# Kernel tuning notes

Hardware: AMD Instinct MI355X
Metric: run time of the kernel (lower is better)

Reference implementation:

```python
import jax, jax.numpy as jnp
import numpy as np

B, N, D = 4, 4096, 256

def setup_inputs() -> dict:
    key = jax.random.key(0)
    k1, = jax.random.split(key, 1)
    x = jax.random.normal(k1, (B, N, D), dtype=jnp.float32)
    attn_mask = jnp.ones((B, 1, N), dtype=jnp.int32)
    pad_mask = jnp.ones((B, 1, N), dtype=jnp.int32)
    return {"x": x, "attn_mask": attn_mask, "pad_mask": pad_mask, "dim_": D}

def reference(x, attn_mask, pad_mask, dim_):
    # adj is None -> scores = x @ x^T / sqrt(d)
    scale = jnp.sqrt(jnp.asarray(x.shape[-1], x.dtype))
    scores = jnp.einsum('bnd,bmd->bnm', x, x) / scale  # [B, N, N]
    # NOTE: original calls non-in-place masked_fill and discards the result,
    # so pad_mask / attn_mask have no effect on the output (faithful).
    prob = jax.nn.softmax(scores, axis=-1)
    # dropout is identity in inference mode
    return jnp.einsum('bnm,bmd->bnd', prob, x)
```

## Files before the change

### kernel.cpp

```cpp
#include <hip/hip_runtime.h>

typedef __attribute__((ext_vector_type(8))) short short8;
typedef __attribute__((ext_vector_type(4))) float f32x4;
typedef __attribute__((ext_vector_type(4))) unsigned int u32x4;

#define NTOK 4096
#define DIM  256
#define P_STRIDE 72
#define TILE_ELEMS 32768

__device__ __forceinline__ unsigned pack2bf(float a, float b) {
  unsigned ua = __builtin_bit_cast(unsigned, a) + 0x8000u;
  unsigned ub = __builtin_bit_cast(unsigned, b) + 0x8000u;
  return __builtin_amdgcn_perm(ub, ua, 0x07060302u);
}

__global__ __launch_bounds__(256, 4)
void prep_kernel(const float* __restrict__ X, unsigned short* __restrict__ Img) {
  __shared__ __align__(16) unsigned short rowbf[8 * 256];
  const int b    = blockIdx.x & 3;
  const int sub  = blockIdx.x >> 2;
  const int t    = sub >> 3;
  const int part = sub & 7;
  const int tid  = threadIdx.x;
  const float* src = X + ((size_t)b * NTOK + t * 64 + part * 8) * DIM;
  unsigned short* dst = Img + ((size_t)(b * 64 + t)) * TILE_ELEMS;
  {
    const int r = tid >> 5;
    const int c = tid & 31;
    const float* s = src + r * DIM + c * 8;
    f32x4 f0 = *(const f32x4*)s;
    f32x4 f1 = *(const f32x4*)(s + 4);
    union { unsigned u[4]; u32x4 v; } p;
    p.u[0] = pack2bf(f0[0], f0[1]);
    p.u[1] = pack2bf(f0[2], f0[3]);
    p.u[2] = pack2bf(f1[0], f1[1]);
    p.u[3] = pack2bf(f1[2], f1[3]);
    const int gr = part * 8 + r;
    *(u32x4*)(dst + gr * 256 + ((c ^ (gr & 7)) << 3)) = p.v;
    *(u32x4*)(&rowbf[r * 256 + c * 8]) = p.v;
  }
  __syncthreads();
  {
    const int d = tid;
    union { unsigned short s[8]; u32x4 v; } p;
    #pragma unroll
    for (int i = 0; i < 8; ++i) p.s[i] = rowbf[i * 256 + d];
    *(u32x4*)(dst + 16384 + part * 2048 + d * 8) = p.v;
  }
}

__device__ __forceinline__ void pv_reg(const unsigned short* __restrict__ pr,
                                       const short8 (&bv)[2][4],
                                       f32x4 (&o)[2][4],
                                       int qh, int quad, int ln) {
  #pragma unroll
  for (int ks = 0; ks < 2; ++ks) {
    const int pos = (ks * 4 + quad) ^ ((ln >> 3) << 1);
    short8 ap[2];
    #pragma unroll
    for (int s = 0; s < 2; ++s)
      ap[s] = *(const short8*)(&pr[(qh * 32 + s * 16 + ln) * P_STRIDE + (pos << 3)]);
    #pragma unroll
    for (int s = 0; s < 2; ++s)
      #pragma unroll
      for (int dt = 0; dt < 4; ++dt)
        o[s][dt] = __builtin_amdgcn_mfma_f32_16x16x32_bf16(ap[s], bv[ks][dt], o[s][dt], 0, 0, 0);
  }
}

__global__ __launch_bounds__(512, 1)
void fa_kernel(const unsigned short* __restrict__ Img, float* __restrict__ Out) {
  __shared__ __align__(16) unsigned short ksb[2][16384];
  __shared__ __align__(16) unsigned short pb[2][64 * P_STRIDE];
  __shared__ float lbuf[64][4];

  const int tid  = threadIdx.x;
  const int b    = blockIdx.x & 3;
  const int qblk = blockIdx.x >> 2;
  const int wave = tid >> 6;
  const int lane = tid & 63;
  const int ln   = lane & 15;
  const int quad = lane >> 4;
  const int swz  = ln & 7;
  const int qh   = wave & 1;
  const int role = wave >> 1;

  const unsigned short* imgb  = Img + (size_t)b * 64 * TILE_ELEMS;
  const char*           imgbc = (const char*)imgb;

  short8 aQ[2][8];
  #pragma unroll
  for (int s = 0; s < 2; ++s) {
    const unsigned short* qrow =
        imgb + (size_t)qblk * TILE_ELEMS + (qh * 32 + s * 16 + ln) * 256;
    #pragma unroll
    for (int ds = 0; ds < 8; ++ds)
      aQ[s][ds] = *(const short8*)(qrow + (((ds * 4 + quad) ^ swz) << 3));
  }

  f32x4 o[2][4];
  #pragma unroll
  for (int s = 0; s < 2; ++s)
    #pragma unroll
    for (int dt = 0; dt < 4; ++dt) o[s][dt] = (f32x4)(0.0f);
  float lrow[2][4] = {{0.f,0.f,0.f,0.f},{0.f,0.f,0.f,0.f}};

  const float c2 = 0.0901684400f;

  const int pwPos = ((role * 2 + (ln >> 3)) ^ ((quad >> 1) << 1)) << 3;
  const int pwCol = ln & 7;

  const char* gK = imgbc + (size_t)wave * 4096 + (size_t)lane * 16;
  #pragma unroll
  for (int i = 0; i < 4; ++i)
    __builtin_amdgcn_global_load_lds(
        (const __attribute__((address_space(1))) unsigned*)(gK + i * 1024),
        (__attribute__((address_space(3))) unsigned*)(&ksb[0][wave * 2048 + i * 512]),
        16, 0, 0);

  const unsigned short* ktg = imgb + 16384 + (size_t)quad * 2048 + (role * 64 + ln) * 8;

  short8 bvE[2][4];
  short8 bvO[2][4];

  auto iter = [&](int t, short8 (&bvLd)[2][4], short8 (&bvUs)[2][4],
                  bool doPV) __attribute__((always_inline)) {
    __syncthreads();
    const int buf = t & 1;

    if (t < 63) {
      const char* g = gK + (size_t)(t + 1) * 65536;
      unsigned short* l = &ksb[buf ^ 1][wave * 2048];
      #pragma unroll
      for (int i = 0; i < 4; ++i)
        __builtin_amdgcn_global_load_lds(
            (const __attribute__((address_space(1))) unsigned*)(g + i * 1024),
            (__attribute__((address_space(3))) unsigned*)(l + i * 512),
            16, 0, 0);
    }

    {
      const unsigned short* kt = ktg + (size_t)t * TILE_ELEMS;
      #pragma unroll
      for (int ks = 0; ks < 2; ++ks)
        #pragma unroll
        for (int dt = 0; dt < 4; ++dt)
          bvLd[ks][dt] = *(const short8*)(kt + ks * 8192 + dt * 128);
    }

    f32x4 sf0 = (f32x4)(0.0f), sf1 = (f32x4)(0.0f);
    {
      const unsigned short* krow = &ksb[buf][(role * 16 + ln) * 256];
      #pragma unroll
      for (int ds = 0; ds < 8; ++ds) {
        short8 bk = *(const short8*)(krow + (((ds * 4 + quad) ^ swz) << 3));
        sf0 = __builtin_amdgcn_mfma_f32_16x16x32_bf16(aQ[0][ds], bk, sf0, 0, 0, 0);
        sf1 = __builtin_amdgcn_mfma_f32_16x16x32_bf16(aQ[1][ds], bk, sf1, 0, 0, 0);
      }
    }

    unsigned pd0[4], pd1[4];
    #pragma unroll
    for (int j = 0; j < 4; ++j) {
      float p0 = __builtin_amdgcn_exp2f(sf0[j] * c2);
      float p1 = __builtin_amdgcn_exp2f(sf1[j] * c2);
      lrow[0][j] += p0;
      lrow[1][j] += p1;
      unsigned q0 = __builtin_bit_cast(unsigned, p0);
      unsigned q1 = __builtin_bit_cast(unsigned, p1);
      unsigned n0 = (unsigned)__builtin_amdgcn_mov_dpp((int)q0, 0xB1, 0xF, 0xF, true);
      unsigned n1 = (unsigned)__builtin_amdgcn_mov_dpp((int)q1, 0xB1, 0xF, 0xF, true);
      pd0[j] = pack2bf(__builtin_bit_cast(float, q0), __builtin_bit_cast(float, n0));
      pd1[j] = pack2bf(__builtin_bit_cast(float, q1), __builtin_bit_cast(float, n1));
    }

    if (doPV)
      pv_reg(pb[buf ^ 1], bvUs, o, qh, quad, ln);

    if ((ln & 1) == 0) {
      unsigned short* pw = pb[buf];
      #pragma unroll
      for (int j = 0; j < 4; ++j) {
        const int r0 = qh * 32 + quad * 4 + j;
        *(unsigned*)(&pw[r0 * P_STRIDE + pwPos + pwCol]) = pd0[j];
        *(unsigned*)(&pw[(r0 + 16) * P_STRIDE + pwPos + pwCol]) = pd1[j];
      }
    }
  };

  iter(0, bvE, bvO, false);
  #pragma unroll 1
  for (int tt = 1; tt < 63; tt += 2) {
    iter(tt, bvO, bvE, true);
    iter(tt + 1, bvE, bvO, true);
  }
  iter(63, bvO, bvE, true);

  __syncthreads();
  pv_reg(pb[1], bvO, o, qh, quad, ln);

  #pragma unroll
  for (int off = 1; off < 16; off <<= 1)
    #pragma unroll
    for (int s = 0; s < 2; ++s)
      #pragma unroll
      for (int j = 0; j < 4; ++j)
        lrow[s][j] += __shfl_xor(lrow[s][j], off, 64);
  if (ln == 0) {
    #pragma unroll
    for (int s = 0; s < 2; ++s)
      #pragma unroll
      for (int j = 0; j < 4; ++j)
        lbuf[qh * 32 + s * 16 + quad * 4 + j][role] = lrow[s][j];
  }
  __syncthreads();

  #pragma unroll
  for (int s = 0; s < 2; ++s) {
    float* outp = Out + (size_t)(b * NTOK + qblk * 64 + qh * 32 + s * 16) * DIM + role * 64;
    #pragma unroll
    for (int j = 0; j < 4; ++j) {
      const int row = s * 16 + quad * 4 + j;
      f32x4 lv = *(const f32x4*)lbuf[qh * 32 + row];
      const float rl = 1.0f / (lv[0] + lv[1] + lv[2] + lv[3]);
      #pragma unroll
      for (int dt = 0; dt < 4; ++dt)
        outp[(size_t)(quad * 4 + j) * DIM + dt * 16 + ln] = o[s][dt][j] * rl;
    }
  }
}

extern "C" void kernel_launch(void* const* d_in, const int* in_sizes, int n_in,
                              void* d_out, int out_size, void* d_ws, size_t ws_size,
                              hipStream_t stream) {
  const float* X = (const float*)d_in[0];
  float* Out = (float*)d_out;
  unsigned short* Img = (unsigned short*)d_ws;
  (void)in_sizes; (void)n_in; (void)out_size; (void)ws_size;
  hipLaunchKernelGGL(prep_kernel, dim3(2048), dim3(256), 0, stream, X, Img);
  hipLaunchKernelGGL(fa_kernel, dim3(256), dim3(512), 0, stream, Img, Out);
}
```

Measured before the change: 166.3 us.

## Specialize waves into QK/softmax producers and PV consumers

Result: no change. 163.4 us (-1.8%).

```diff
diff --git a/kernel.cpp b/kernel.cpp
--- a/kernel.cpp
+++ b/kernel.cpp
@@ -50,24 +50,84 @@
   }
 }
 
-__device__ __forceinline__ void pv_reg(const unsigned short* __restrict__ pr,
-                                       const short8 (&bv)[2][4],
-                                       f32x4 (&o)[2][4],
-                                       int qh, int quad, int ln) {
-  #pragma unroll
-  for (int ks = 0; ks < 2; ++ks) {
-    const int pos = (ks * 4 + quad) ^ ((ln >> 3) << 1);
-    short8 ap[2];
-    #pragma unroll
-    for (int s = 0; s < 2; ++s)
-      ap[s] = *(const short8*)(&pr[(qh * 32 + s * 16 + ln) * P_STRIDE + (pos << 3)]);
-    #pragma unroll
-    for (int s = 0; s < 2; ++s)
-      #pragma unroll
-      for (int dt = 0; dt < 4; ++dt)
-        o[s][dt] = __builtin_amdgcn_mfma_f32_16x16x32_bf16(ap[s], bv[ks][dt], o[s][dt], 0, 0, 0);
-  }
-}
+#define FA_STEP(T, VLD, VUS)                                                   \
+  {                                                                            \
+    const int t_ = (T);                                                        \
+    __syncthreads();                                                           \
+    const int buf_ = t_ & 1;                                                   \
+    if (!isQK) {                                                               \
+      if (t_ < 63) {                                                           \
+        const char* g = gK + (size_t)(t_ + 1) * 65536;                         \
+        unsigned short* l = &ksb[buf_ ^ 1][role * 4096];                       \
+        _Pragma("unroll")                                                      \
+        for (int i = 0; i < 8; ++i)                                            \
+          __builtin_amdgcn_global_load_lds(                                    \
+              (const __attribute__((address_space(1))) unsigned*)(g + i*1024), \
+              (__attribute__((address_space(3))) unsigned*)(l + i*512),        \
+              16, 0, 0);                                                       \
+      }                                                                        \
+      {                                                                        \
+        const unsigned short* vt = vtg + (size_t)t_ * TILE_ELEMS;              \
+        _Pragma("unroll")                                                      \
+        for (int ks = 0; ks < 2; ++ks)                                         \
+          _Pragma("unroll")                                                    \
+          for (int dt = 0; dt < 4; ++dt)                                       \
+            u[(VLD) + ks * 4 + dt] = __builtin_bit_cast(f32x4,                 \
+                *(const short8*)(vt + (ks * 4 + quad) * 2048 + dt * 128));     \
+      }                                                                        \
+      if (t_ > 0) {                                                            \
+        const unsigned short* prd = pb[buf_ ^ 1];                              \
+        _Pragma("unroll")                                                      \
+        for (int ks = 0; ks < 2; ++ks) {                                       \
+          const int pos = (ks * 4 + quad) ^ ((ln >> 3) << 1);                  \
+          _Pragma("unroll")                                                    \
+          for (int s = 0; s < 4; ++s) {                                        \
+            short8 ap = *(const short8*)(                                      \
+                &prd[(s * 16 + ln) * P_STRIDE + (pos << 3)]);                  \
+            _Pragma("unroll")                                                  \
+            for (int dt = 0; dt < 4; ++dt)                                     \
+              u[s * 4 + dt] = __builtin_amdgcn_mfma_f32_16x16x32_bf16(         \
+                  ap, __builtin_bit_cast(short8, u[(VUS) + ks * 4 + dt]),      \
+                  u[s * 4 + dt], 0, 0, 0);                                     \
+          }                                                                    \
+        }                                                                      \
+      }                                                                        \
+    } else {                                                                   \
+      const unsigned short* krow = &ksb[buf_][(role * 16 + ln) * 256];         \
+      f32x4 sf[4];                                                             \
+      _Pragma("unroll")                                                        \
+      for (int s = 0; s < 4; ++s) sf[s] = (f32x4)(0.0f);                       \
+      _Pragma("unroll")                                                        \
+      for (int ds = 0; ds < 8; ++ds) {                                         \
+        short8 bk = *(const short8*)(krow + (((ds * 4 + quad) ^ swz) << 3));   \
+        _Pragma("unroll")                                                      \
+        for (int s = 0; s < 4; ++s)                                            \
+          sf[s] = __builtin_amdgcn_mfma_f32_16x16x32_bf16(                     \
+              __builtin_bit_cast(short8, u[s * 8 + ds]), bk, sf[s], 0, 0, 0);  \
+      }                                                                        \
+      unsigned pd[4][4];                                                       \
+      _Pragma("unroll")                                                        \
+      for (int s = 0; s < 4; ++s)                                              \
+        _Pragma("unroll")                                                      \
+        for (int j = 0; j < 4; ++j) {                                          \
+          float p0 = __builtin_amdgcn_exp2f(sf[s][j] * c2);                    \
+          lrow[s][j] += p0;                                                    \
+          unsigned q0 = __builtin_bit_cast(unsigned, p0);                      \
+          unsigned n0 = (unsigned)__builtin_amdgcn_mov_dpp((int)q0, 0xB1,      \
+                                                           0xF, 0xF, true);   \
+          pd[s][j] = pack2bf(p0, __builtin_bit_cast(float, n0));               \
+        }                                                                      \
+      if ((ln & 1) == 0) {                                                     \
+        unsigned short* pw = pb[buf_];                                         \
+        _Pragma("unroll")                                                      \
+        for (int s = 0; s < 4; ++s)                                            \
+          _Pragma("unroll")                                                    \
+          for (int j = 0; j < 4; ++j)                                          \
+            *(unsigned*)(&pw[(s * 16 + quad * 4 + j) * P_STRIDE +              \
+                             pwPos + pwCol]) = pd[s][j];                       \
+      }                                                                        \
+    }                                                                          \
+  }
 
 __global__ __launch_bounds__(512, 1)
 void fa_kernel(const unsigned short* __restrict__ Img, float* __restrict__ Out) {
@@ -83,150 +143,100 @@
   const int ln   = lane & 15;
   const int quad = lane >> 4;
   const int swz  = ln & 7;
-  const int qh   = wave & 1;
-  const int role = wave >> 1;
+  const bool isQK = wave < 4;
+  const int  role = wave & 3;
 
   const unsigned short* imgb  = Img + (size_t)b * 64 * TILE_ELEMS;
   const char*           imgbc = (const char*)imgb;
 
-  short8 aQ[2][8];
-  #pragma unroll
-  for (int s = 0; s < 2; ++s) {
-    const unsigned short* qrow =
-        imgb + (size_t)qblk * TILE_ELEMS + (qh * 32 + s * 16 + ln) * 256;
-    #pragma unroll
-    for (int ds = 0; ds < 8; ++ds)
-      aQ[s][ds] = *(const short8*)(qrow + (((ds * 4 + quad) ^ swz) << 3));
-  }
-
-  f32x4 o[2][4];
-  #pragma unroll
-  for (int s = 0; s < 2; ++s)
-    #pragma unroll
-    for (int dt = 0; dt < 4; ++dt) o[s][dt] = (f32x4)(0.0f);
-  float lrow[2][4] = {{0.f,0.f,0.f,0.f},{0.f,0.f,0.f,0.f}};
-
   const float c2 = 0.0901684400f;
 
   const int pwPos = ((role * 2 + (ln >> 3)) ^ ((quad >> 1) << 1)) << 3;
   const int pwCol = ln & 7;
 
-  const char* gK = imgbc + (size_t)wave * 4096 + (size_t)lane * 16;
-  #pragma unroll
-  for (int i = 0; i < 4; ++i)
-    __builtin_amdgcn_global_load_lds(
-        (const __attribute__((address_space(1))) unsigned*)(gK + i * 1024),
-        (__attribute__((address_space(3))) unsigned*)(&ksb[0][wave * 2048 + i * 512]),
-        16, 0, 0);
-
-  const unsigned short* ktg = imgb + 16384 + (size_t)quad * 2048 + (role * 64 + ln) * 8;
-
-  short8 bvE[2][4];
-  short8 bvO[2][4];
-
-  auto iter = [&](int t, short8 (&bvLd)[2][4], short8 (&bvUs)[2][4],
-                  bool doPV) __attribute__((always_inline)) {
-    __syncthreads();
-    const int buf = t & 1;
-
-    if (t < 63) {
-      const char* g = gK + (size_t)(t + 1) * 65536;
-      unsigned short* l = &ksb[buf ^ 1][wave * 2048];
-      #pragma unroll
-      for (int i = 0; i < 4; ++i)
-        __builtin_amdgcn_global_load_lds(
-            (const __attribute__((address_space(1))) unsigned*)(g + i * 1024),
-            (__attribute__((address_space(3))) unsigned*)(l + i * 512),
-            16, 0, 0);
-    }
-
-    {
-      const unsigned short* kt = ktg + (size_t)t * TILE_ELEMS;
-      #pragma unroll
-      for (int ks = 0; ks < 2; ++ks)
-        #pragma unroll
-        for (int dt = 0; dt < 4; ++dt)
-          bvLd[ks][dt] = *(const short8*)(kt + ks * 8192 + dt * 128);
-    }
-
-    f32x4 sf0 = (f32x4)(0.0f), sf1 = (f32x4)(0.0f);
-    {
-      const unsigned short* krow = &ksb[buf][(role * 16 + ln) * 256];
-      #pragma unroll
-      for (int ds = 0; ds < 8; ++ds) {
-        short8 bk = *(const short8*)(krow + (((ds * 4 + quad) ^ swz) << 3));
-        sf0 = __builtin_amdgcn_mfma_f32_16x16x32_bf16(aQ[0][ds], bk, sf0, 0, 0, 0);
-        sf1 = __builtin_amdgcn_mfma_f32_16x16x32_bf16(aQ[1][ds], bk, sf1, 0, 0, 0);
-      }
-    }
-
-    unsigned pd0[4], pd1[4];
-    #pragma unroll
-    for (int j = 0; j < 4; ++j) {
-      float p0 = __builtin_amdgcn_exp2f(sf0[j] * c2);
-      float p1 = __builtin_amdgcn_exp2f(sf1[j] * c2);
-      lrow[0][j] += p0;
-      lrow[1][j] += p1;
-      unsigned q0 = __builtin_bit_cast(unsigned, p0);
-      unsigned q1 = __builtin_bit_cast(unsigned, p1);
-      unsigned n0 = (unsigned)__builtin_amdgcn_mov_dpp((int)q0, 0xB1, 0xF, 0xF, true);
-      unsigned n1 = (unsigned)__builtin_amdgcn_mov_dpp((int)q1, 0xB1, 0xF, 0xF, true);
-      pd0[j] = pack2bf(__builtin_bit_cast(float, q0), __builtin_bit_cast(float, n0));
-      pd1[j] = pack2bf(__builtin_bit_cast(float, q1), __builtin_bit_cast(float, n1));
-    }
-
-    if (doPV)
-      pv_reg(pb[buf ^ 1], bvUs, o, qh, quad, ln);
-
-    if ((ln & 1) == 0) {
-      unsigned short* pw = pb[buf];
-      #pragma unroll
-      for (int j = 0; j < 4; ++j) {
-        const int r0 = qh * 32 + quad * 4 + j;
-        *(unsigned*)(&pw[r0 * P_STRIDE + pwPos + pwCol]) = pd0[j];
-        *(unsigned*)(&pw[(r0 + 16) * P_STRIDE + pwPos + pwCol]) = pd1[j];
-      }
-    }
-  };
-
-  iter(0, bvE, bvO, false);
+  const char* gK = imgbc + (size_t)role * 8192 + (size_t)lane * 16;
+  const unsigned short* vtg = imgb + 16384 + (size_t)(role * 64 + ln) * 8;
+
+  float lrow[4][4] = {{0,0,0,0},{0,0,0,0},{0,0,0,0},{0,0,0,0}};
+
+  f32x4 u[32];
+  if (isQK) {
+    #pragma unroll
+    for (int s = 0; s < 4; ++s) {
+      const unsigned short* qrow =
+          imgb + (size_t)qblk * TILE_ELEMS + (s * 16 + ln) * 256;
+      #pragma unroll
+      for (int ds = 0; ds < 8; ++ds)
+        u[s * 8 + ds] = __builtin_bit_cast(f32x4,
+            *(const short8*)(qrow + (((ds * 4 + quad) ^ swz) << 3)));
+    }
+  } else {
+    #pragma unroll
+    for (int i = 0; i < 16; ++i) u[i] = (f32x4)(0.0f);
+    #pragma unroll
+    for (int i = 0; i < 8; ++i)
+      __builtin_amdgcn_global_load_lds(
+          (const __attribute__((address_space(1))) unsigned*)(gK + i * 1024),
+          (__attribute__((address_space(3))) unsigned*)(&ksb[0][role * 4096 + i * 512]),
+          16, 0, 0);
+  }
+
+  FA_STEP(0, 16, 24);
   #pragma unroll 1
   for (int tt = 1; tt < 63; tt += 2) {
-    iter(tt, bvO, bvE, true);
-    iter(tt + 1, bvE, bvO, true);
-  }
-  iter(63, bvO, bvE, true);
+    FA_STEP(tt, 24, 16);
+    FA_STEP(tt + 1, 16, 24);
+  }
+  FA_STEP(63, 24, 16);
 
   __syncthreads();
-  pv_reg(pb[1], bvO, o, qh, quad, ln);
-
-  #pragma unroll
-  for (int off = 1; off < 16; off <<= 1)
-    #pragma unroll
-    for (int s = 0; s < 2; ++s)
-      #pragma unroll
-      for (int j = 0; j < 4; ++j)
-        lrow[s][j] += __shfl_xor(lrow[s][j], off, 64);
-  if (ln == 0) {
-    #pragma unroll
-    for (int s = 0; s < 2; ++s)
-      #pragma unroll
-      for (int j = 0; j < 4; ++j)
-        lbuf[qh * 32 + s * 16 + quad * 4 + j][role] = lrow[s][j];
+
+  if (isQK) {
+    #pragma unroll
+    for (int off = 1; off < 16; off <<= 1)
+      #pragma unroll
+      for (int s = 0; s < 4; ++s)
+        #pragma unroll
+        for (int j = 0; j < 4; ++j)
+          lrow[s][j] += __shfl_xor(lrow[s][j], off, 64);
+    if (ln == 0) {
+      #pragma unroll
+      for (int s = 0; s < 4; ++s)
+        #pragma unroll
+        for (int j = 0; j < 4; ++j)
+          lbuf[s * 16 + quad * 4 + j][role] = lrow[s][j];
+    }
+  } else {
+    const unsigned short* prd = pb[1];
+    #pragma unroll
+    for (int ks = 0; ks < 2; ++ks) {
+      const int pos = (ks * 4 + quad) ^ ((ln >> 3) << 1);
+      #pragma unroll
+      for (int s = 0; s < 4; ++s) {
+        short8 ap = *(const short8*)(&prd[(s * 16 + ln) * P_STRIDE + (pos << 3)]);
+        #pragma unroll
+        for (int dt = 0; dt < 4; ++dt)
+          u[s * 4 + dt] = __builtin_amdgcn_mfma_f32_16x16x32_bf16(
+              ap, __builtin_bit_cast(short8, u[24 + ks * 4 + dt]),
+              u[s * 4 + dt], 0, 0, 0);
+      }
+    }
   }
   __syncthreads();
 
-  #pragma unroll
-  for (int s = 0; s < 2; ++s) {
-    float* outp = Out + (size_t)(b * NTOK + qblk * 64 + qh * 32 + s * 16) * DIM + role * 64;
-    #pragma unroll
-    for (int j = 0; j < 4; ++j) {
-      const int row = s * 16 + quad * 4 + j;
-      f32x4 lv = *(const f32x4*)lbuf[qh * 32 + row];
-      const float rl = 1.0f / (lv[0] + lv[1] + lv[2] + lv[3]);
-      #pragma unroll
-      for (int dt = 0; dt < 4; ++dt)
-        outp[(size_t)(quad * 4 + j) * DIM + dt * 16 + ln] = o[s][dt][j] * rl;
+  if (!isQK) {
+    float* outB = Out + (size_t)(b * NTOK + qblk * 64) * DIM + role * 64;
+    #pragma unroll
+    for (int s = 0; s < 4; ++s) {
+      #pragma unroll
+      for (int j = 0; j < 4; ++j) {
+        const int row = s * 16 + quad * 4 + j;
+        f32x4 lv = *(const f32x4*)lbuf[row];
+        const float rl = 1.0f / (lv[0] + lv[1] + lv[2] + lv[3]);
+        #pragma unroll
+        for (int dt = 0; dt < 4; ++dt)
+          outB[(size_t)row * DIM + dt * 16 + ln] = u[s * 4 + dt][j] * rl;
+      }
     }
   }
 }
```
